# Performance work log

Measured on AMD Instinct MI355X. Metric: run time of the kernel, lower is better.

The kernel has to match this reference:

```python
import jax, jax.numpy as jnp
import numpy as np

B, HF, WF = 64, 14, 14
E, D, H, EM, V, L = 2048, 256, 256, 256, 10000, 32


def setup_inputs() -> dict:
    key = jax.random.key(0)
    ks = jax.random.split(key, 16)
    s = lambda k, shape: jax.random.normal(k, shape, jnp.float32) * 0.02
    lengths = jnp.clip(jax.random.randint(ks[2], (B, 1), 2, L + 1), 2, L)
    lengths = lengths.at[0, 0].set(L)  # ensure max target length == L-1 (static)
    return {
        "image_feature": jax.random.normal(ks[0], (B, HF, WF, E), jnp.float32),
        "caption_token": jax.random.randint(ks[1], (B, L), 0, V),
        "caption_length": lengths,
        "Wf": s(ks[3], (E, H)), "bf": jnp.zeros((H,), jnp.float32),
        "Wh": s(ks[4], (D, H)), "bh": jnp.zeros((H,), jnp.float32),
        "We": s(ks[5], (H, 1)), "be": jnp.zeros((1,), jnp.float32),
        "emb": jax.random.uniform(ks[6], (V, EM), jnp.float32, -0.1, 0.1),
        "W_ih": s(ks[7], (EM + E, 4 * D)), "b_ih": jnp.zeros((4 * D,), jnp.float32),
        "W_hh": s(ks[8], (D, 4 * D)), "b_hh": jnp.zeros((4 * D,), jnp.float32),
        "W_hid": s(ks[9], (E, D)), "b_hid": jnp.zeros((D,), jnp.float32),
        "W_cell": s(ks[10], (E, D)), "b_cell": jnp.zeros((D,), jnp.float32),
        "W_gate": s(ks[11], (D, E)), "b_gate": jnp.zeros((E,), jnp.float32),
        "W_head": jax.random.uniform(ks[12], (D, V), jnp.float32, -0.1, 0.1),
        "b_head": jnp.zeros((V,), jnp.float32),
    }


def reference(image_feature, caption_token, caption_length,
              Wf, bf, Wh, bh, We, be, emb,
              W_ih, b_ih, W_hh, b_hh,
              W_hid, b_hid, W_cell, b_cell,
              W_gate, b_gate, W_head, b_head):
    feat = image_feature.reshape(image_feature.shape[0], -1, image_feature.shape[-1])  # [B,P,E]
    lengths = caption_length[:, 0]
    order = jnp.argsort(-lengths)               # descending, stable
    feat = feat[order]
    tok = caption_token[order]
    target = lengths[order] - 1                 # [B] target lengths
    T = tok.shape[1] - 1                        # static max target length

    mean_feat = feat.mean(axis=1)               # [B,E]
    h0 = mean_feat @ W_hid + b_hid              # init hidden
    c0 = mean_feat @ W_cell + b_cell            # init cell
    cap_emb = emb[tok]                          # [B,L,EM] teacher-forcing embeds
    fe = feat @ Wf + bf                         # [B,P,H] feature proj (loop-invariant)

    def step(carry, t):
        h, c = carry
        m = (target > t)[:, None].astype(h.dtype)        # active-row mask (block_size)
        # additive attention
        he = (h @ Wh + bh)[:, None, :]                   # [B,1,H]
        e = jax.nn.relu(fe + he) @ We + be               # [B,P,1]
        w = jax.nn.softmax(e, axis=1)                    # over pixels
        ctx = (w * feat).sum(axis=1)                     # [B,E]
        # sigmoid gate on context
        ctx = jax.nn.sigmoid(h @ W_gate + b_gate) * ctx
        # LSTMCell (torch gate order i,f,g,o)
        x = jnp.concatenate([cap_emb[:, t], ctx], axis=1)
        g = x @ W_ih + b_ih + h @ W_hh + b_hh
        i, f, gg, o = jnp.split(g, 4, axis=1)
        c_new = jax.nn.sigmoid(f) * c + jax.nn.sigmoid(i) * jnp.tanh(gg)
        h_new = jax.nn.sigmoid(o) * jnp.tanh(c_new)
        pred = h_new @ W_head + b_head                   # dropout = identity (eval)
        h = jnp.where(m > 0, h_new, h)
        c = jnp.where(m > 0, c_new, c)
        return (h, c), (pred * m, w[:, :, 0] * m)

    _, (preds, weights) = jax.lax.scan(step, (h0, c0), jnp.arange(T))
    caption_prediction = jnp.transpose(preds, (1, 0, 2))   # [B,T,V]
    attention_weight = jnp.transpose(weights, (1, 0, 2))   # [B,T,P]
    return caption_prediction, attention_weight
```

## Files before the change

kernel.cpp:

```cpp
#include <hip/hip_runtime.h>
#include <math.h>

#define B 64
#define P 196
#define E 2048
#define D 256
#define H_ 256
#define EM 256
#define V 10000
#define L 32
#define T 31
#define KX 2560

__global__ __launch_bounds__(64) void sort_kernel(const int* __restrict__ clen,
                                                  int* __restrict__ order,
                                                  int* __restrict__ target) {
    __shared__ int len_s[B];
    int i = threadIdx.x;
    len_s[i] = clen[i];
    __syncthreads();
    int li = len_s[i];
    int rank = 0;
    for (int j = 0; j < B; ++j) {
        int lj = len_s[j];
        if (lj > li || (lj == li && j < i)) rank++;
    }
    order[rank] = i;
    target[rank] = li - 1;
}

__global__ __launch_bounds__(256) void mean_kernel(const float* __restrict__ feat,
                                                   const int* __restrict__ order,
                                                   float* __restrict__ mean_feat) {
    int b = blockIdx.x;
    int e = blockIdx.y * 256 + threadIdx.x;
    int src = order[b];
    const float* fp = feat + (size_t)src * P * E + e;
    float acc = 0.f;
    #pragma unroll 4
    for (int p = 0; p < P; ++p) acc += fp[(size_t)p * E];
    mean_feat[b * E + e] = acc * (1.0f / (float)P);
}

__global__ __launch_bounds__(256) void h0c0_gemm(const float* __restrict__ mean_feat,
                                                 const float* __restrict__ W_hid,
                                                 const float* __restrict__ W_cell,
                                                 float* __restrict__ hpart) {
    __shared__ float As[32][68];
    __shared__ float Bs[32][64];
    int cb = blockIdx.x;
    int ky = blockIdx.y;
    int tid = threadIdx.x;
    int tx = tid & 15, ty = tid >> 4;
    const float* Wsrc;
    int ncol0;
    if (cb < 4) { Wsrc = W_hid;  ncol0 = cb * 64; }
    else        { Wsrc = W_cell; ncol0 = (cb - 4) * 64; }
    float acc[4][4] = {};
    for (int k0 = ky * 256; k0 < ky * 256 + 256; k0 += 32) {
        #pragma unroll
        for (int q = 0; q < 2; ++q) {
            int idx = q * 256 + tid;
            int kv = idx & 7, m = idx >> 3;
            float4 v = *(const float4*)(mean_feat + (size_t)m * E + k0 + kv * 4);
            As[kv * 4 + 0][m] = v.x;
            As[kv * 4 + 1][m] = v.y;
            As[kv * 4 + 2][m] = v.z;
            As[kv * 4 + 3][m] = v.w;
        }
        #pragma unroll
        for (int q = 0; q < 2; ++q) {
            int idx = q * 256 + tid;
            int n4 = idx & 15, kk = idx >> 4;
            float4 v = *(const float4*)(Wsrc + (size_t)(k0 + kk) * 256 + ncol0 + n4 * 4);
            *(float4*)&Bs[kk][n4 * 4] = v;
        }
        __syncthreads();
        #pragma unroll
        for (int kk = 0; kk < 32; ++kk) {
            float4 av = *(const float4*)&As[kk][ty * 4];
            float4 bv = *(const float4*)&Bs[kk][tx * 4];
            acc[0][0] += av.x * bv.x; acc[0][1] += av.x * bv.y; acc[0][2] += av.x * bv.z; acc[0][3] += av.x * bv.w;
            acc[1][0] += av.y * bv.x; acc[1][1] += av.y * bv.y; acc[1][2] += av.y * bv.z; acc[1][3] += av.y * bv.w;
            acc[2][0] += av.z * bv.x; acc[2][1] += av.z * bv.y; acc[2][2] += av.z * bv.z; acc[2][3] += av.z * bv.w;
            acc[3][0] += av.w * bv.x; acc[3][1] += av.w * bv.y; acc[3][2] += av.w * bv.z; acc[3][3] += av.w * bv.w;
        }
        __syncthreads();
    }
    #pragma unroll
    for (int a = 0; a < 4; ++a) {
        int row = ty * 4 + a;
        float4 o = {acc[a][0], acc[a][1], acc[a][2], acc[a][3]};
        *(float4*)(hpart + ((size_t)ky * B + row) * 512 + cb * 64 + tx * 4) = o;
    }
}

__global__ __launch_bounds__(256) void h0c0_reduce(const float* __restrict__ hpart,
                                                   const float* __restrict__ b_hid,
                                                   const float* __restrict__ b_cell,
                                                   const float* __restrict__ emb,
                                                   const int* __restrict__ cap_tok,
                                                   const int* __restrict__ order,
                                                   float* __restrict__ h,
                                                   float* __restrict__ c0,
                                                   float* __restrict__ xbuf) {
    int b = blockIdx.x, tid = threadIdx.x;
    float s0 = 0.f, s1 = 0.f;
    #pragma unroll
    for (int ky = 0; ky < 8; ++ky) {
        const float* hp = hpart + ((size_t)ky * B + b) * 512;
        s0 += hp[tid];
        s1 += hp[256 + tid];
    }
    float h0 = s0 + b_hid[tid];
    h[b * D + tid] = h0;
    c0[b * D + tid] = s1 + b_cell[tid];
    xbuf[(size_t)b * KX + 2304 + tid] = h0;
    int tok0 = cap_tok[order[b] * L + 0];
    xbuf[(size_t)b * KX + tid] = emb[(size_t)tok0 * EM + tid];
}

__global__ __launch_bounds__(256) void fe_gemm(const float* __restrict__ feat,
                                               const int* __restrict__ order,
                                               const float* __restrict__ Wf,
                                               const float* __restrict__ bf,
                                               float* __restrict__ fe) {
    __shared__ float As[32][68];
    __shared__ float Bs[32][64];
    __shared__ int srcRow[64];
    int rowBlock = blockIdx.x;
    int colBlock = blockIdx.y;
    int tid = threadIdx.x;
    if (tid < 64) {
        int gr = rowBlock * 64 + tid;
        int b = gr / P, p = gr % P;
        srcRow[tid] = order[b] * P + p;
    }
    __syncthreads();
    int tx = tid & 15, ty = tid >> 4;
    float acc[4][4] = {};
    for (int k0 = 0; k0 < E; k0 += 32) {
        #pragma unroll
        for (int q = 0; q < 2; ++q) {
            int idx = q * 256 + tid;
            int kv = idx & 7, m = idx >> 3;
            float4 v = *(const float4*)(feat + (size_t)srcRow[m] * E + k0 + kv * 4);
            As[kv * 4 + 0][m] = v.x;
            As[kv * 4 + 1][m] = v.y;
            As[kv * 4 + 2][m] = v.z;
            As[kv * 4 + 3][m] = v.w;
        }
        {
            int n4 = tid & 15, kk = tid >> 4;
            float4 v = *(const float4*)(Wf + (size_t)(k0 + kk) * H_ + colBlock * 64 + n4 * 4);
            *(float4*)&Bs[kk][n4 * 4] = v;
            int kk2 = kk + 16;
            float4 v2 = *(const float4*)(Wf + (size_t)(k0 + kk2) * H_ + colBlock * 64 + n4 * 4);
            *(float4*)&Bs[kk2][n4 * 4] = v2;
        }
        __syncthreads();
        #pragma unroll
        for (int kk = 0; kk < 32; ++kk) {
            float4 av = *(const float4*)&As[kk][ty * 4];
            float4 bv = *(const float4*)&Bs[kk][tx * 4];
            acc[0][0] += av.x * bv.x; acc[0][1] += av.x * bv.y; acc[0][2] += av.x * bv.z; acc[0][3] += av.x * bv.w;
            acc[1][0] += av.y * bv.x; acc[1][1] += av.y * bv.y; acc[1][2] += av.y * bv.z; acc[1][3] += av.y * bv.w;
            acc[2][0] += av.z * bv.x; acc[2][1] += av.z * bv.y; acc[2][2] += av.z * bv.z; acc[2][3] += av.z * bv.w;
            acc[3][0] += av.w * bv.x; acc[3][1] += av.w * bv.y; acc[3][2] += av.w * bv.z; acc[3][3] += av.w * bv.w;
        }
        __syncthreads();
    }
    float4 bias = *(const float4*)(bf + colBlock * 64 + tx * 4);
    #pragma unroll
    for (int a = 0; a < 4; ++a) {
        int gr = rowBlock * 64 + ty * 4 + a;
        float4 o;
        o.x = acc[a][0] + bias.x;
        o.y = acc[a][1] + bias.y;
        o.z = acc[a][2] + bias.z;
        o.w = acc[a][3] + bias.w;
        *(float4*)(fe + (size_t)gr * H_ + colBlock * 64 + tx * 4) = o;
    }
}

__global__ __launch_bounds__(256) void attn_ctx(const int* __restrict__ target,
                                                const float* __restrict__ gpart,
                                                const float* __restrict__ b_ih,
                                                const float* __restrict__ b_hh,
                                                const float* __restrict__ emb,
                                                const int* __restrict__ cap_tok,
                                                const int* __restrict__ order,
                                                const float* __restrict__ Wh,
                                                const float* __restrict__ bh,
                                                const float* __restrict__ We,
                                                const float* __restrict__ be,
                                                const float* __restrict__ fe,
                                                const float* __restrict__ h0,
                                                const float* __restrict__ c_rd,
                                                float* __restrict__ c_wr,
                                                float* __restrict__ hn_all,
                                                float* __restrict__ xbuf,
                                                float* __restrict__ out2,
                                                const float* __restrict__ feat,
                                                const float* __restrict__ W_gate,
                                                const float* __restrict__ b_gate,
                                                int t) {
    int b = blockIdx.x, y = blockIdx.y, tid = threadIdx.x;
    int tgt = target[b];
    bool pw_active = (t > 0) && (tgt > t - 1);
    bool at_active = (tgt > t);
    if (!at_active && !(pw_active && y == 0)) return;

    __shared__ float hs[D];
    __shared__ float hes[D];
    __shared__ float es[200];
    __shared__ float red[4];
    __shared__ float4 rc[3][64];
    __shared__ float4 rg[3][64];

    if (pw_active) {
        int d = tid;
        float gi = b_ih[d] + b_hh[d];
        float gf = b_ih[D + d] + b_hh[D + d];
        float gg = b_ih[2 * D + d] + b_hh[2 * D + d];
        float go = b_ih[3 * D + d] + b_hh[3 * D + d];
        #pragma unroll
        for (int ky = 0; ky < 8; ++ky) {
            const float* gp = gpart + ((size_t)ky * B + b) * 1024;
            gi += gp[d];
            gf += gp[D + d];
            gg += gp[2 * D + d];
            go += gp[3 * D + d];
        }
        float c_old = c_rd[b * D + d];
        float si = 1.f / (1.f + expf(-gi));
        float sf = 1.f / (1.f + expf(-gf));
        float so = 1.f / (1.f + expf(-go));
        float cn = sf * c_old + si * tanhf(gg);
        float hnv = so * tanhf(cn);
        hs[d] = hnv;
        if (y == 0) {
            c_wr[b * D + d] = cn;
            hn_all[((size_t)(t - 1) * B + b) * D + d] = hnv;
            xbuf[(size_t)b * KX + 2304 + d] = hnv;
            int tokn = cap_tok[order[b] * L + t];
            xbuf[(size_t)b * KX + d] = emb[(size_t)tokn * EM + d];
        }
    } else {
        hs[tid] = h0[b * D + tid];
    }
    __syncthreads();
    if (!at_active) return;

    {
        float acc = 0.f;
        #pragma unroll 8
        for (int k = 0; k < D; ++k) acc += hs[k] * Wh[(size_t)k * H_ + tid];
        hes[tid] = acc + bh[tid];
    }
    __syncthreads();

    int wave = tid >> 6, lane = tid & 63;
    {
        float4 he4 = *(const float4*)&hes[lane * 4];
        float4 we4 = *(const float4*)(We + lane * 4);
        for (int p = wave; p < P; p += 4) {
            float4 fv = *(const float4*)(fe + ((size_t)b * P + p) * H_ + lane * 4);
            float x0 = fv.x + he4.x; x0 = x0 > 0.f ? x0 : 0.f;
            float x1 = fv.y + he4.y; x1 = x1 > 0.f ? x1 : 0.f;
            float x2 = fv.z + he4.z; x2 = x2 > 0.f ? x2 : 0.f;
            float x3 = fv.w + he4.w; x3 = x3 > 0.f ? x3 : 0.f;
            float s = x0 * we4.x + x1 * we4.y + x2 * we4.z + x3 * we4.w;
            #pragma unroll
            for (int off = 32; off > 0; off >>= 1) s += __shfl_down(s, off);
            if (lane == 0) es[p] = s + be[0];
        }
    }
    __syncthreads();

    {
        float mx = -1e30f;
        for (int p = tid; p < P; p += 256) mx = fmaxf(mx, es[p]);
        #pragma unroll
        for (int off = 32; off > 0; off >>= 1) mx = fmaxf(mx, __shfl_down(mx, off));
        if (lane == 0) red[wave] = mx;
        __syncthreads();
        mx = fmaxf(fmaxf(red[0], red[1]), fmaxf(red[2], red[3]));
        __syncthreads();
        float sum = 0.f;
        for (int p = tid; p < P; p += 256) {
            float ex = expf(es[p] - mx);
            es[p] = ex;
            sum += ex;
        }
        #pragma unroll
        for (int off = 32; off > 0; off >>= 1) sum += __shfl_down(sum, off);
        if (lane == 0) red[wave] = sum;
        __syncthreads();
        sum = red[0] + red[1] + red[2] + red[3];
        float inv = 1.0f / sum;
        for (int p = tid; p < P; p += 256) {
            float wv = es[p] * inv;
            es[p] = wv;
            if (y == 0) out2[((size_t)b * T + t) * P + p] = wv;
        }
    }
    __syncthreads();

    {
        int c4 = tid & 63, q = tid >> 6;
        int src = order[b];
        const float4* f4 = (const float4*)(feat + (size_t)src * P * E) + y * 64 + c4;
        float4 acc = {0.f, 0.f, 0.f, 0.f};
        for (int p = q * 49; p < q * 49 + 49; ++p) {
            float w = es[p];
            float4 fv = f4[(size_t)p * 512];
            acc.x += w * fv.x; acc.y += w * fv.y; acc.z += w * fv.z; acc.w += w * fv.w;
        }
        const float4* g4 = (const float4*)W_gate + y * 64 + c4;
        float4 gacc = {0.f, 0.f, 0.f, 0.f};
        for (int k = q * 64; k < q * 64 + 64; ++k) {
            float hv = hs[k];
            float4 wv = g4[(size_t)k * 512];
            gacc.x += hv * wv.x; gacc.y += hv * wv.y; gacc.z += hv * wv.z; gacc.w += hv * wv.w;
        }
        if (q) { rc[q - 1][c4] = acc; rg[q - 1][c4] = gacc; }
        __syncthreads();
        if (q == 0) {
            #pragma unroll
            for (int j = 0; j < 3; ++j) {
                float4 a = rc[j][c4], g = rg[j][c4];
                acc.x += a.x; acc.y += a.y; acc.z += a.z; acc.w += a.w;
                gacc.x += g.x; gacc.y += g.y; gacc.z += g.z; gacc.w += g.w;
            }
            float4 gb = *(const float4*)(b_gate + (y * 64 + c4) * 4);
            float4 o;
            o.x = acc.x / (1.f + expf(-(gacc.x + gb.x)));
            o.y = acc.y / (1.f + expf(-(gacc.y + gb.y)));
            o.z = acc.z / (1.f + expf(-(gacc.z + gb.z)));
            o.w = acc.w / (1.f + expf(-(gacc.w + gb.w)));
            *(float4*)(xbuf + (size_t)b * KX + EM + (y * 64 + c4) * 4) = o;
        }
    }
}

__global__ __launch_bounds__(256) void pw_final(const int* __restrict__ target,
                                                const float* __restrict__ gpart,
                                                const float* __restrict__ b_ih,
                                                const float* __restrict__ b_hh,
                                                const float* __restrict__ c_rd,
                                                float* __restrict__ hn_all) {
    int b = blockIdx.x;
    if (target[b] < T) return;
    int d = threadIdx.x;
    float gi = b_ih[d] + b_hh[d];
    float gf = b_ih[D + d] + b_hh[D + d];
    float gg = b_ih[2 * D + d] + b_hh[2 * D + d];
    float go = b_ih[3 * D + d] + b_hh[3 * D + d];
    #pragma unroll
    for (int ky = 0; ky < 8; ++ky) {
        const float* gp = gpart + ((size_t)ky * B + b) * 1024;
        gi += gp[d];
        gf += gp[D + d];
        gg += gp[2 * D + d];
        go += gp[3 * D + d];
    }
    float c_old = c_rd[b * D + d];
    float si = 1.f / (1.f + expf(-gi));
    float sf = 1.f / (1.f + expf(-gf));
    float so = 1.f / (1.f + expf(-go));
    float cn = sf * c_old + si * tanhf(gg);
    float hnv = so * tanhf(cn);
    hn_all[((size_t)(T - 1) * B + b) * D + d] = hnv;
}

__global__ __launch_bounds__(256) void lstm_gemm(const float* __restrict__ xbuf,
                                                 const float* __restrict__ W_ih,
                                                 const float* __restrict__ W_hh,
                                                 float* __restrict__ gpart) {
    __shared__ float As[32][68];
    __shared__ float Bs[32][64];
    int cb = blockIdx.x;
    int ky = blockIdx.y;
    int tid = threadIdx.x;
    int tx = tid & 15, ty = tid >> 4;
    float acc[4][4] = {};
    int k0base = ky * 320;
    for (int k0 = k0base; k0 < k0base + 320; k0 += 32) {
        #pragma unroll
        for (int q = 0; q < 2; ++q) {
            int idx = q * 256 + tid;
            int kv = idx & 7, m = idx >> 3;
            float4 v = *(const float4*)(xbuf + (size_t)m * KX + k0 + kv * 4);
            As[kv * 4 + 0][m] = v.x;
            As[kv * 4 + 1][m] = v.y;
            As[kv * 4 + 2][m] = v.z;
            As[kv * 4 + 3][m] = v.w;
        }
        #pragma unroll
        for (int q = 0; q < 2; ++q) {
            int idx = q * 256 + tid;
            int n4 = idx & 15, kk = idx >> 4;
            int k = k0 + kk;
            const float* src = (k < EM + E) ? (W_ih + (size_t)k * 1024)
                                            : (W_hh + (size_t)(k - EM - E) * 1024);
            float4 v = *(const float4*)(src + cb * 64 + n4 * 4);
            *(float4*)&Bs[kk][n4 * 4] = v;
        }
        __syncthreads();
        #pragma unroll
        for (int kk = 0; kk < 32; ++kk) {
            float4 av = *(const float4*)&As[kk][ty * 4];
            float4 bv = *(const float4*)&Bs[kk][tx * 4];
            acc[0][0] += av.x * bv.x; acc[0][1] += av.x * bv.y; acc[0][2] += av.x * bv.z; acc[0][3] += av.x * bv.w;
            acc[1][0] += av.y * bv.x; acc[1][1] += av.y * bv.y; acc[1][2] += av.y * bv.z; acc[1][3] += av.y * bv.w;
            acc[2][0] += av.z * bv.x; acc[2][1] += av.z * bv.y; acc[2][2] += av.z * bv.z; acc[2][3] += av.z * bv.w;
            acc[3][0] += av.w * bv.x; acc[3][1] += av.w * bv.y; acc[3][2] += av.w * bv.z; acc[3][3] += av.w * bv.w;
        }
        __syncthreads();
    }
    #pragma unroll
    for (int a = 0; a < 4; ++a) {
        int bidx = ty * 4 + a;
        float4 o = {acc[a][0], acc[a][1], acc[a][2], acc[a][3]};
        *(float4*)(gpart + ((size_t)ky * B + bidx) * 1024 + cb * 64 + tx * 4) = o;
    }
}

__global__ __launch_bounds__(256) void head_batch(const float* __restrict__ hn_all,
                                                  const float* __restrict__ W_head,
                                                  const float* __restrict__ b_head,
                                                  const int* __restrict__ target,
                                                  float* __restrict__ out1) {
    int by = blockIdx.y;
    int t = by >> 1, qh = by & 1;
    if (target[qh * 32] <= t) return;
    __shared__ float hs[32][260];
    int cb = blockIdx.x;
    int tid = threadIdx.x;
    #pragma unroll
    for (int q = 0; q < 8; ++q) {
        int idx = q * 256 + tid;
        int r = idx >> 6, kq = idx & 63;
        float4 v = *(const float4*)(hn_all + ((size_t)t * B + qh * 32 + r) * D + kq * 4);
        *(float4*)&hs[r][kq * 4] = v;
    }
    __syncthreads();
    int col = cb * 64 + (tid & 63);
    int rgrp = (tid >> 6) * 8;
    if (col < V) {
        float acc[8] = {};
        for (int kq = 0; kq < 64; ++kq) {
            float w0 = W_head[(size_t)(kq * 4 + 0) * V + col];
            float w1 = W_head[(size_t)(kq * 4 + 1) * V + col];
            float w2 = W_head[(size_t)(kq * 4 + 2) * V + col];
            float w3 = W_head[(size_t)(kq * 4 + 3) * V + col];
            #pragma unroll
            for (int r = 0; r < 8; ++r) {
                float4 hv = *(const float4*)&hs[rgrp + r][kq * 4];
                acc[r] += hv.x * w0 + hv.y * w1 + hv.z * w2 + hv.w * w3;
            }
        }
        float bh_ = b_head[col];
        #pragma unroll
        for (int r = 0; r < 8; ++r) {
            int brow = qh * 32 + rgrp + r;
            if (target[brow] > t)
                out1[((size_t)brow * T + t) * V + col] = acc[r] + bh_;
        }
    }
}

extern "C" void kernel_launch(void* const* d_in, const int* in_sizes, int n_in,
                              void* d_out, int out_size, void* d_ws, size_t ws_size,
                              hipStream_t stream) {
    const float* feat   = (const float*)d_in[0];
    const int*   tok    = (const int*)d_in[1];
    const int*   clen   = (const int*)d_in[2];
    const float* Wf     = (const float*)d_in[3];
    const float* bf     = (const float*)d_in[4];
    const float* Wh     = (const float*)d_in[5];
    const float* bh     = (const float*)d_in[6];
    const float* We     = (const float*)d_in[7];
    const float* be     = (const float*)d_in[8];
    const float* emb    = (const float*)d_in[9];
    const float* W_ih   = (const float*)d_in[10];
    const float* b_ih   = (const float*)d_in[11];
    const float* W_hh   = (const float*)d_in[12];
    const float* b_hh   = (const float*)d_in[13];
    const float* W_hid  = (const float*)d_in[14];
    const float* b_hid  = (const float*)d_in[15];
    const float* W_cell = (const float*)d_in[16];
    const float* b_cell = (const float*)d_in[17];
    const float* W_gate = (const float*)d_in[18];
    const float* b_gate = (const float*)d_in[19];
    const float* W_head = (const float*)d_in[20];
    const float* b_head = (const float*)d_in[21];

    float* out1 = (float*)d_out;
    float* out2 = out1 + (size_t)B * T * V;

    char* wp = (char*)d_ws;
    int* order   = (int*)wp;           wp += 256;
    int* targetp = (int*)wp;           wp += 256;
    float* fe    = (float*)wp;         wp += (size_t)B * P * H_ * sizeof(float);
    float* hbuf  = (float*)wp;         wp += (size_t)B * D * sizeof(float);
    float* cbuf  = (float*)wp;         wp += (size_t)2 * B * D * sizeof(float);
    float* xbuf  = (float*)wp;         wp += (size_t)B * KX * sizeof(float);
    float* gpart = (float*)wp;         wp += (size_t)8 * B * 1024 * sizeof(float);
    float* mean_feat = (float*)wp;     wp += (size_t)B * E * sizeof(float);
    float* hpart = (float*)wp;         wp += (size_t)8 * B * 512 * sizeof(float);
    float* hn_all = (float*)wp;        wp += (size_t)T * B * D * sizeof(float);

    hipMemsetAsync(d_out, 0, (size_t)out_size * sizeof(float), stream);

    sort_kernel<<<1, 64, 0, stream>>>(clen, order, targetp);
    mean_kernel<<<dim3(B, E / 256), 256, 0, stream>>>(feat, order, mean_feat);
    h0c0_gemm<<<dim3(8, 8), 256, 0, stream>>>(mean_feat, W_hid, W_cell, hpart);
    h0c0_reduce<<<B, 256, 0, stream>>>(hpart, b_hid, b_cell, emb, tok, order,
                                       hbuf, cbuf, xbuf);
    fe_gemm<<<dim3(196, 4), 256, 0, stream>>>(feat, order, Wf, bf, fe);

    for (int t = 0; t < T; ++t) {
        attn_ctx<<<dim3(B, 8), 256, 0, stream>>>(targetp, gpart, b_ih, b_hh, emb, tok,
                                                 order, Wh, bh, We, be, fe, hbuf,
                                                 cbuf + (size_t)((t + 1) & 1) * B * D,
                                                 cbuf + (size_t)(t & 1) * B * D,
                                                 hn_all, xbuf, out2,
                                                 feat, W_gate, b_gate, t);
        lstm_gemm<<<dim3(16, 8), 256, 0, stream>>>(xbuf, W_ih, W_hh, gpart);
    }
    pw_final<<<B, 256, 0, stream>>>(targetp, gpart, b_ih, b_hh, cbuf, hn_all);

    head_batch<<<dim3(157, 62), 256, 0, stream>>>(hn_all, W_head, b_head, targetp, out1);
}
```

Measured before the change: 2.732 ms.

## Precompute embedding gate GEMM, split-K fe and LSTM GEMMs, batch head over timesteps

Hoists the teacher-forced embedding part of the LSTM input projection out of the time loop into one batched GEMM over all timesteps (Gemb), which shrinks the per-step K from 2560 to 2304. It also raises the per-step LSTM GEMM split-K to 18 chunks, splits the fe GEMM along K with a separate reduce kernel, and makes the head kernel loop over 8 timesteps per block so the launch grid is smaller. Scratch buffers are placed inside the output region, and the output is zeroed just before the head kernel writes it. The attention Wh matvec is unrolled into four accumulators. The trade is extra partial-sum reads per step and more memory traffic for the fe reduce.

```diff
diff --git a/kernel.cpp b/kernel.cpp
--- a/kernel.cpp
+++ b/kernel.cpp
@@ -10,7 +10,8 @@
 #define V 10000
 #define L 32
 #define T 31
-#define KX 2560
+#define KX2 2304
+#define NKY 18
 
 __global__ __launch_bounds__(64) void sort_kernel(const int* __restrict__ clen,
                                                   int* __restrict__ order,
@@ -98,9 +99,6 @@
 __global__ __launch_bounds__(256) void h0c0_reduce(const float* __restrict__ hpart,
                                                    const float* __restrict__ b_hid,
                                                    const float* __restrict__ b_cell,
-                                                   const float* __restrict__ emb,
-                                                   const int* __restrict__ cap_tok,
-                                                   const int* __restrict__ order,
                                                    float* __restrict__ h,
                                                    float* __restrict__ c0,
                                                    float* __restrict__ xbuf) {
@@ -115,21 +113,73 @@
     float h0 = s0 + b_hid[tid];
     h[b * D + tid] = h0;
     c0[b * D + tid] = s1 + b_cell[tid];
-    xbuf[(size_t)b * KX + 2304 + tid] = h0;
-    int tok0 = cap_tok[order[b] * L + 0];
-    xbuf[(size_t)b * KX + tid] = emb[(size_t)tok0 * EM + tid];
+    xbuf[(size_t)b * KX2 + 2048 + tid] = h0;
+}
+
+__global__ __launch_bounds__(256) void gemb_gemm(const float* __restrict__ emb,
+                                                 const int* __restrict__ cap_tok,
+                                                 const int* __restrict__ order,
+                                                 const float* __restrict__ W_ih,
+                                                 float* __restrict__ Gemb) {
+    __shared__ float As[32][68];
+    __shared__ float Bs[32][64];
+    __shared__ int srcTok[64];
+    int cb = blockIdx.x;
+    int t  = blockIdx.y;
+    int tid = threadIdx.x;
+    if (tid < 64) srcTok[tid] = cap_tok[order[tid] * L + t];
+    __syncthreads();
+    int tx = tid & 15, ty = tid >> 4;
+    float acc[4][4] = {};
+    for (int k0 = 0; k0 < EM; k0 += 32) {
+        #pragma unroll
+        for (int q = 0; q < 2; ++q) {
+            int idx = q * 256 + tid;
+            int kv = idx & 7, m = idx >> 3;
+            float4 v = *(const float4*)(emb + (size_t)srcTok[m] * EM + k0 + kv * 4);
+            As[kv * 4 + 0][m] = v.x;
+            As[kv * 4 + 1][m] = v.y;
+            As[kv * 4 + 2][m] = v.z;
+            As[kv * 4 + 3][m] = v.w;
+        }
+        #pragma unroll
+        for (int q = 0; q < 2; ++q) {
+            int idx = q * 256 + tid;
+            int n4 = idx & 15, kk = idx >> 4;
+            float4 v = *(const float4*)(W_ih + (size_t)(k0 + kk) * 1024 + cb * 64 + n4 * 4);
+            *(float4*)&Bs[kk][n4 * 4] = v;
+        }
+        __syncthreads();
+        #pragma unroll
+        for (int kk = 0; kk < 32; ++kk) {
+            float4 av = *(const float4*)&As[kk][ty * 4];
+            float4 bv = *(const float4*)&Bs[kk][tx * 4];
+            acc[0][0] += av.x * bv.x; acc[0][1] += av.x * bv.y; acc[0][2] += av.x * bv.z; acc[0][3] += av.x * bv.w;
+            acc[1][0] += av.y * bv.x; acc[1][1] += av.y * bv.y; acc[1][2] += av.y * bv.z; acc[1][3] += av.y * bv.w;
+            acc[2][0] += av.z * bv.x; acc[2][1] += av.z * bv.y; acc[2][2] += av.z * bv.z; acc[2][3] += av.z * bv.w;
+            acc[3][0] += av.w * bv.x; acc[3][1] += av.w * bv.y; acc[3][2] += av.w * bv.z; acc[3][3] += av.w * bv.w;
+        }
+        __syncthreads();
+    }
+    #pragma unroll
+    for (int a = 0; a < 4; ++a) {
+        int row = ty * 4 + a;
+        float4 o = {acc[a][0], acc[a][1], acc[a][2], acc[a][3]};
+        *(float4*)(Gemb + ((size_t)t * B + row) * 1024 + cb * 64 + tx * 4) = o;
+    }
 }
 
 __global__ __launch_bounds__(256) void fe_gemm(const float* __restrict__ feat,
                                                const int* __restrict__ order,
                                                const float* __restrict__ Wf,
-                                               const float* __restrict__ bf,
-                                               float* __restrict__ fe) {
+                                               float* __restrict__ dst0,
+                                               float* __restrict__ dst1) {
     __shared__ float As[32][68];
     __shared__ float Bs[32][64];
     __shared__ int srcRow[64];
     int rowBlock = blockIdx.x;
     int colBlock = blockIdx.y;
+    int kz = blockIdx.z;
     int tid = threadIdx.x;
     if (tid < 64) {
         int gr = rowBlock * 64 + tid;
@@ -139,7 +189,7 @@
     __syncthreads();
     int tx = tid & 15, ty = tid >> 4;
     float acc[4][4] = {};
-    for (int k0 = 0; k0 < E; k0 += 32) {
+    for (int k0 = kz * 1024; k0 < kz * 1024 + 1024; k0 += 32) {
         #pragma unroll
         for (int q = 0; q < 2; ++q) {
             int idx = q * 256 + tid;
@@ -170,25 +220,33 @@
         }
         __syncthreads();
     }
-    float4 bias = *(const float4*)(bf + colBlock * 64 + tx * 4);
+    float* dst = kz ? dst1 : dst0;
     #pragma unroll
     for (int a = 0; a < 4; ++a) {
         int gr = rowBlock * 64 + ty * 4 + a;
-        float4 o;
-        o.x = acc[a][0] + bias.x;
-        o.y = acc[a][1] + bias.y;
-        o.z = acc[a][2] + bias.z;
-        o.w = acc[a][3] + bias.w;
-        *(float4*)(fe + (size_t)gr * H_ + colBlock * 64 + tx * 4) = o;
-    }
+        float4 o = {acc[a][0], acc[a][1], acc[a][2], acc[a][3]};
+        *(float4*)(dst + (size_t)gr * H_ + colBlock * 64 + tx * 4) = o;
+    }
+}
+
+__global__ __launch_bounds__(256) void fe_reduce(float* __restrict__ fe,
+                                                 const float* __restrict__ fepart1,
+                                                 const float* __restrict__ bf) {
+    size_t f4 = (size_t)blockIdx.x * 256 + threadIdx.x;
+    int col4 = (int)(f4 & 63);
+    float4 a = *(const float4*)(fe + f4 * 4);
+    float4 b = *(const float4*)(fepart1 + f4 * 4);
+    float4 bias = *(const float4*)(bf + col4 * 4);
+    float4 o = {a.x + b.x + bias.x, a.y + b.y + bias.y,
+                a.z + b.z + bias.z, a.w + b.w + bias.w};
+    *(float4*)(fe + f4 * 4) = o;
 }
 
 __global__ __launch_bounds__(256) void attn_ctx(const int* __restrict__ target,
                                                 const float* __restrict__ gpart,
+                                                const float* __restrict__ Gemb,
                                                 const float* __restrict__ b_ih,
                                                 const float* __restrict__ b_hh,
-                                                const float* __restrict__ emb,
-                                                const int* __restrict__ cap_tok,
                                                 const int* __restrict__ order,
                                                 const float* __restrict__ Wh,
                                                 const float* __restrict__ bh,
@@ -220,12 +278,13 @@
 
     if (pw_active) {
         int d = tid;
-        float gi = b_ih[d] + b_hh[d];
-        float gf = b_ih[D + d] + b_hh[D + d];
-        float gg = b_ih[2 * D + d] + b_hh[2 * D + d];
-        float go = b_ih[3 * D + d] + b_hh[3 * D + d];
-        #pragma unroll
-        for (int ky = 0; ky < 8; ++ky) {
+        const float* ge = Gemb + ((size_t)(t - 1) * B + b) * 1024;
+        float gi = b_ih[d] + b_hh[d] + ge[d];
+        float gf = b_ih[D + d] + b_hh[D + d] + ge[D + d];
+        float gg = b_ih[2 * D + d] + b_hh[2 * D + d] + ge[2 * D + d];
+        float go = b_ih[3 * D + d] + b_hh[3 * D + d] + ge[3 * D + d];
+        #pragma unroll
+        for (int ky = 0; ky < NKY; ++ky) {
             const float* gp = gpart + ((size_t)ky * B + b) * 1024;
             gi += gp[d];
             gf += gp[D + d];
@@ -242,9 +301,7 @@
         if (y == 0) {
             c_wr[b * D + d] = cn;
             hn_all[((size_t)(t - 1) * B + b) * D + d] = hnv;
-            xbuf[(size_t)b * KX + 2304 + d] = hnv;
-            int tokn = cap_tok[order[b] * L + t];
-            xbuf[(size_t)b * KX + d] = emb[(size_t)tokn * EM + d];
+            xbuf[(size_t)b * KX2 + 2048 + d] = hnv;
         }
     } else {
         hs[tid] = h0[b * D + tid];
@@ -253,10 +310,15 @@
     if (!at_active) return;
 
     {
-        float acc = 0.f;
-        #pragma unroll 8
-        for (int k = 0; k < D; ++k) acc += hs[k] * Wh[(size_t)k * H_ + tid];
-        hes[tid] = acc + bh[tid];
+        float a0 = 0.f, a1 = 0.f, a2 = 0.f, a3 = 0.f;
+        #pragma unroll 4
+        for (int k = 0; k < D; k += 4) {
+            a0 += hs[k]     * Wh[(size_t)k * H_ + tid];
+            a1 += hs[k + 1] * Wh[(size_t)(k + 1) * H_ + tid];
+            a2 += hs[k + 2] * Wh[(size_t)(k + 2) * H_ + tid];
+            a3 += hs[k + 3] * Wh[(size_t)(k + 3) * H_ + tid];
+        }
+        hes[tid] = (a0 + a1) + (a2 + a3) + bh[tid];
     }
     __syncthreads();
 
@@ -277,7 +339,6 @@
         }
     }
     __syncthreads();
-
     {
         float mx = -1e30f;
         for (int p = tid; p < P; p += 256) mx = fmaxf(mx, es[p]);
@@ -339,13 +400,14 @@
             o.y = acc.y / (1.f + expf(-(gacc.y + gb.y)));
             o.z = acc.z / (1.f + expf(-(gacc.z + gb.z)));
             o.w = acc.w / (1.f + expf(-(gacc.w + gb.w)));
-            *(float4*)(xbuf + (size_t)b * KX + EM + (y * 64 + c4) * 4) = o;
+            *(float4*)(xbuf + (size_t)b * KX2 + (y * 64 + c4) * 4) = o;
         }
     }
 }
 
 __global__ __launch_bounds__(256) void pw_final(const int* __restrict__ target,
                                                 const float* __restrict__ gpart,
+                                                const float* __restrict__ Gemb,
                                                 const float* __restrict__ b_ih,
                                                 const float* __restrict__ b_hh,
                                                 const float* __restrict__ c_rd,
@@ -353,12 +415,13 @@
     int b = blockIdx.x;
     if (target[b] < T) return;
     int d = threadIdx.x;
-    float gi = b_ih[d] + b_hh[d];
-    float gf = b_ih[D + d] + b_hh[D + d];
-    float gg = b_ih[2 * D + d] + b_hh[2 * D + d];
-    float go = b_ih[3 * D + d] + b_hh[3 * D + d];
+    const float* ge = Gemb + ((size_t)(T - 1) * B + b) * 1024;
+    float gi = b_ih[d] + b_hh[d] + ge[d];
+    float gf = b_ih[D + d] + b_hh[D + d] + ge[D + d];
+    float gg = b_ih[2 * D + d] + b_hh[2 * D + d] + ge[2 * D + d];
+    float go = b_ih[3 * D + d] + b_hh[3 * D + d] + ge[3 * D + d];
     #pragma unroll
-    for (int ky = 0; ky < 8; ++ky) {
+    for (int ky = 0; ky < NKY; ++ky) {
         const float* gp = gpart + ((size_t)ky * B + b) * 1024;
         gi += gp[d];
         gf += gp[D + d];
@@ -385,13 +448,13 @@
     int tid = threadIdx.x;
     int tx = tid & 15, ty = tid >> 4;
     float acc[4][4] = {};
-    int k0base = ky * 320;
-    for (int k0 = k0base; k0 < k0base + 320; k0 += 32) {
+    int k0base = ky * 128;
+    for (int k0 = k0base; k0 < k0base + 128; k0 += 32) {
         #pragma unroll
         for (int q = 0; q < 2; ++q) {
             int idx = q * 256 + tid;
             int kv = idx & 7, m = idx >> 3;
-            float4 v = *(const float4*)(xbuf + (size_t)m * KX + k0 + kv * 4);
+            float4 v = *(const float4*)(xbuf + (size_t)m * KX2 + k0 + kv * 4);
             As[kv * 4 + 0][m] = v.x;
             As[kv * 4 + 1][m] = v.y;
             As[kv * 4 + 2][m] = v.z;
@@ -402,8 +465,8 @@
             int idx = q * 256 + tid;
             int n4 = idx & 15, kk = idx >> 4;
             int k = k0 + kk;
-            const float* src = (k < EM + E) ? (W_ih + (size_t)k * 1024)
-                                            : (W_hh + (size_t)(k - EM - E) * 1024);
+            const float* src = (k < E) ? (W_ih + (size_t)(EM + k) * 1024)
+                                       : (W_hh + (size_t)(k - E) * 1024);
             float4 v = *(const float4*)(src + cb * 64 + n4 * 4);
             *(float4*)&Bs[kk][n4 * 4] = v;
         }
@@ -433,40 +496,45 @@
                                                   const int* __restrict__ target,
                                                   float* __restrict__ out1) {
     int by = blockIdx.y;
-    int t = by >> 1, qh = by & 1;
-    if (target[qh * 32] <= t) return;
+    int qh = by >> 2, tc = by & 3;
+    int t0 = tc * 8;
+    if (target[qh * 32] <= t0) return;
     __shared__ float hs[32][260];
     int cb = blockIdx.x;
     int tid = threadIdx.x;
-    #pragma unroll
-    for (int q = 0; q < 8; ++q) {
-        int idx = q * 256 + tid;
-        int r = idx >> 6, kq = idx & 63;
-        float4 v = *(const float4*)(hn_all + ((size_t)t * B + qh * 32 + r) * D + kq * 4);
-        *(float4*)&hs[r][kq * 4] = v;
-    }
-    __syncthreads();
     int col = cb * 64 + (tid & 63);
     int rgrp = (tid >> 6) * 8;
-    if (col < V) {
-        float acc[8] = {};
-        for (int kq = 0; kq < 64; ++kq) {
-            float w0 = W_head[(size_t)(kq * 4 + 0) * V + col];
-            float w1 = W_head[(size_t)(kq * 4 + 1) * V + col];
-            float w2 = W_head[(size_t)(kq * 4 + 2) * V + col];
-            float w3 = W_head[(size_t)(kq * 4 + 3) * V + col];
+    float bh_ = (col < V) ? b_head[col] : 0.f;
+    for (int t = t0; t < t0 + 8 && t < T; ++t) {
+        if (target[qh * 32] <= t) break;
+        __syncthreads();
+        #pragma unroll
+        for (int q = 0; q < 8; ++q) {
+            int idx = q * 256 + tid;
+            int r = idx >> 6, kq = idx & 63;
+            float4 v = *(const float4*)(hn_all + ((size_t)t * B + qh * 32 + r) * D + kq * 4);
+            *(float4*)&hs[r][kq * 4] = v;
+        }
+        __syncthreads();
+        if (col < V) {
+            float acc[8] = {};
+            for (int kq = 0; kq < 64; ++kq) {
+                float w0 = W_head[(size_t)(kq * 4 + 0) * V + col];
+                float w1 = W_head[(size_t)(kq * 4 + 1) * V + col];
+                float w2 = W_head[(size_t)(kq * 4 + 2) * V + col];
+                float w3 = W_head[(size_t)(kq * 4 + 3) * V + col];
+                #pragma unroll
+                for (int r = 0; r < 8; ++r) {
+                    float4 hv = *(const float4*)&hs[rgrp + r][kq * 4];
+                    acc[r] += hv.x * w0 + hv.y * w1 + hv.z * w2 + hv.w * w3;
+                }
+            }
             #pragma unroll
             for (int r = 0; r < 8; ++r) {
-                float4 hv = *(const float4*)&hs[rgrp + r][kq * 4];
-                acc[r] += hv.x * w0 + hv.y * w1 + hv.z * w2 + hv.w * w3;
+                int brow = qh * 32 + rgrp + r;
+                if (target[brow] > t)
+                    out1[((size_t)brow * T + t) * V + col] = acc[r] + bh_;
             }
-        }
-        float bh_ = b_head[col];
-        #pragma unroll
-        for (int r = 0; r < 8; ++r) {
-            int brow = qh * 32 + rgrp + r;
-            if (target[brow] > t)
-                out1[((size_t)brow * T + t) * V + col] = acc[r] + bh_;
         }
     }
 }
@@ -506,31 +574,36 @@
     float* fe    = (float*)wp;         wp += (size_t)B * P * H_ * sizeof(float);
     float* hbuf  = (float*)wp;         wp += (size_t)B * D * sizeof(float);
     float* cbuf  = (float*)wp;         wp += (size_t)2 * B * D * sizeof(float);
-    float* xbuf  = (float*)wp;         wp += (size_t)B * KX * sizeof(float);
-    float* gpart = (float*)wp;         wp += (size_t)8 * B * 1024 * sizeof(float);
+    float* xbuf  = (float*)wp;         wp += (size_t)B * KX2 * sizeof(float);
     float* mean_feat = (float*)wp;     wp += (size_t)B * E * sizeof(float);
     float* hpart = (float*)wp;         wp += (size_t)8 * B * 512 * sizeof(float);
     float* hn_all = (float*)wp;        wp += (size_t)T * B * D * sizeof(float);
 
-    hipMemsetAsync(d_out, 0, (size_t)out_size * sizeof(float), stream);
+    float* fepart1 = out1;
+    float* Gemb    = out1 + (size_t)4 * 1024 * 1024;
+    float* gpart   = Gemb + (size_t)T * B * 1024;
+
+    hipMemsetAsync(out2, 0, (size_t)B * T * P * sizeof(float), stream);
 
     sort_kernel<<<1, 64, 0, stream>>>(clen, order, targetp);
     mean_kernel<<<dim3(B, E / 256), 256, 0, stream>>>(feat, order, mean_feat);
     h0c0_gemm<<<dim3(8, 8), 256, 0, stream>>>(mean_feat, W_hid, W_cell, hpart);
-    h0c0_reduce<<<B, 256, 0, stream>>>(hpart, b_hid, b_cell, emb, tok, order,
-                                       hbuf, cbuf, xbuf);
-    fe_gemm<<<dim3(196, 4), 256, 0, stream>>>(feat, order, Wf, bf, fe);
+    h0c0_reduce<<<B, 256, 0, stream>>>(hpart, b_hid, b_cell, hbuf, cbuf, xbuf);
+    fe_gemm<<<dim3(196, 4, 2), 256, 0, stream>>>(feat, order, Wf, fe, fepart1);
+    fe_reduce<<<3136, 256, 0, stream>>>(fe, fepart1, bf);
+    gemb_gemm<<<dim3(16, T), 256, 0, stream>>>(emb, tok, order, W_ih, Gemb);
 
     for (int t = 0; t < T; ++t) {
-        attn_ctx<<<dim3(B, 8), 256, 0, stream>>>(targetp, gpart, b_ih, b_hh, emb, tok,
+        attn_ctx<<<dim3(B, 8), 256, 0, stream>>>(targetp, gpart, Gemb, b_ih, b_hh,
                                                  order, Wh, bh, We, be, fe, hbuf,
                                                  cbuf + (size_t)((t + 1) & 1) * B * D,
                                                  cbuf + (size_t)(t & 1) * B * D,
                                                  hn_all, xbuf, out2,
                                                  feat, W_gate, b_gate, t);
-        lstm_gemm<<<dim3(16, 8), 256, 0, stream>>>(xbuf, W_ih, W_hh, gpart);
-    }
-    pw_final<<<B, 256, 0, stream>>>(targetp, gpart, b_ih, b_hh, cbuf, hn_all);
-
-    head_batch<<<dim3(157, 62), 256, 0, stream>>>(hn_all, W_head, b_head, targetp, out1);
-}
+        lstm_gemm<<<dim3(16, NKY), 256, 0, stream>>>(xbuf, W_ih, W_hh, gpart);
+    }
+    pw_final<<<B, 256, 0, stream>>>(targetp, gpart, Gemb, b_ih, b_hh, cbuf, hn_all);
+
+    hipMemsetAsync(out1, 0, (size_t)B * T * V * sizeof(float), stream);
+    head_batch<<<dim3(157, 8), 256, 0, stream>>>(hn_all, W_head, b_head, targetp, out1);
+}
```

New measurement: 2.628 ms. -3.8%, faster.
